# Kernel optimization log

Measured on AMD Instinct MI355X. Metric: run time of the kernel, lower is better.

Reference implementation:

```python
import jax, jax.numpy as jnp
import numpy as np

D_MODEL, D_STATE, D_CONV, EXPAND = 768, 16, 4, 2
D_INNER = EXPAND * D_MODEL        # 1536
DT_RANK = (D_MODEL + 15) // 16    # 48
B, L = 4, 1024
LN_EPS = 1e-5


def _causal_dw_conv(x, w, b):
    # x: [b,l,d], w: [d,k], b: [d] -- depthwise causal conv along l
    k = w.shape[1]
    xp = jnp.pad(x, ((0, 0), (k - 1, 0), (0, 0)))
    out = jnp.zeros_like(x)
    for i in range(k):  # k = 4, tiny fixed loop
        out = out + xp[:, i:i + x.shape[1], :] * w[:, i]
    return out + b


def _selective_scan(u, delta, A, Bm, Cm, Dp):
    # u, delta: [b,l,d]; A: [d,n]; Bm, Cm: [b,l,n]; Dp: [d]
    def step(h, inp):
        d_t, B_t, C_t, u_t = inp                         # [b,d],[b,n],[b,n],[b,d]
        dA = jnp.exp(d_t[:, :, None] * A)                # [b,d,n]
        h = dA * h + (d_t * u_t)[:, :, None] * B_t[:, None, :]
        return h, jnp.einsum('bdn,bn->bd', h, C_t)
    b, l, d = u.shape
    h0 = jnp.zeros((b, d, A.shape[1]), u.dtype)
    xs = (jnp.swapaxes(delta, 0, 1), jnp.swapaxes(Bm, 0, 1),
          jnp.swapaxes(Cm, 0, 1), jnp.swapaxes(u, 0, 1))
    _, ys = jax.lax.scan(step, h0, xs)                   # ys: [l,b,d]
    return jnp.swapaxes(ys, 0, 1) + u * Dp


def _mamba_dir(xz, conv_w, conv_bias, xp_w, dtp_w, dtp_bias, A_log, Dp):
    x, z = jnp.split(xz, 2, axis=-1)                     # each [b,l,d_inner]
    x = jax.nn.silu(_causal_dw_conv(x, conv_w, conv_bias))
    x_dbl = x @ xp_w.T                                   # [b,l,R+2N]
    dt, Bm, Cm = jnp.split(x_dbl, [DT_RANK, DT_RANK + D_STATE], axis=-1)
    dt = jax.nn.softplus(dt @ dtp_w.T + dtp_bias)        # [b,l,d_inner]
    A = -jnp.exp(A_log)                                  # [d_inner,n]
    y = _selective_scan(x, dt, A, Bm, Cm, Dp)
    return y * jax.nn.silu(z)


def _block_single(h, ln_w, ln_b, in_w, conv_w, conv_bias, xp_w, dtp_w, dtp_bias,
                  A_log, D_p, conv_w_b, conv_bias_b, xp_w_b, dtp_w_b, dtp_bias_b,
                  A_b_log, D_b, out_w):
    # LayerNorm
    mu = jnp.mean(h, -1, keepdims=True)
    var = jnp.mean(jnp.square(h - mu), -1, keepdims=True)
    hn = (h - mu) * jax.lax.rsqrt(var + LN_EPS) * ln_w + ln_b
    # Mamba (bimamba v2): shared in_proj/out_proj, fwd + flipped bwd scan
    xz = hn @ in_w.T                                     # [b,l,2*d_inner]
    out_f = _mamba_dir(xz, conv_w, conv_bias, xp_w, dtp_w, dtp_bias, A_log, D_p)
    out_b = _mamba_dir(xz[:, ::-1], conv_w_b, conv_bias_b, xp_w_b, dtp_w_b,
                       dtp_bias_b, A_b_log, D_b)
    return (out_f + out_b[:, ::-1]) @ out_w.T            # [b,l,d_model]


def setup_inputs() -> dict:
    key = jax.random.key(0)
    ks = iter(jax.random.split(key, 40))
    f = lambda *s: jax.random.normal(next(ks), s, jnp.float32)
    p = {}
    p['h_r'] = f(B, L, D_MODEL)
    p['h_i'] = f(B, L, D_MODEL)
    # leading axis 2 = (real-branch mamba_r, imag-branch mamba_i) parameters
    p['ln_w'] = jnp.ones((2, D_MODEL), jnp.float32)
    p['ln_b'] = jnp.zeros((2, D_MODEL), jnp.float32)
    p['in_w'] = f(2, 2 * D_INNER, D_MODEL) * 0.02
    a_init = jnp.broadcast_to(jnp.log(jnp.arange(1, D_STATE + 1, dtype=jnp.float32)),
                              (2, D_INNER, D_STATE))
    for pre in ('', 'b_'):
        sfx = '_b' if pre else ''
        p['conv_w' + sfx] = f(2, D_INNER, D_CONV) * 0.2
        p['conv_bias' + sfx] = f(2, D_INNER) * 0.02
        p['xp_w' + sfx] = f(2, DT_RANK + 2 * D_STATE, D_INNER) * 0.02
        p['dtp_w' + sfx] = f(2, D_INNER, DT_RANK) * 0.1
        p['dtp_bias' + sfx] = f(2, D_INNER) * 0.5
        p['A_log' + sfx if not pre else 'A_b_log'] = a_init
        p['D_p' + sfx if not pre else 'D_b'] = f(2, D_INNER) * 0.1
    p['out_w'] = f(2, D_MODEL, D_INNER) * 0.02
    return p


def reference(h_r, h_i, ln_w, ln_b, in_w, conv_w, conv_bias, xp_w, dtp_w,
              dtp_bias, A_log, D_p, conv_w_b, conv_bias_b, xp_w_b, dtp_w_b,
              dtp_bias_b, A_b_log, D_b, out_w):
    h = jnp.stack([h_r, h_i])                            # [2,b,l,d_model]
    out = jax.vmap(_block_single)(h, ln_w, ln_b, in_w, conv_w, conv_bias, xp_w,
                                  dtp_w, dtp_bias, A_log, D_p, conv_w_b,
                                  conv_bias_b, xp_w_b, dtp_w_b, dtp_bias_b,
                                  A_b_log, D_b, out_w)
    return (out[0], out[1])
```

## Files before the change

kernel.cpp:

```cpp
#include <hip/hip_runtime.h>
#include <hip/hip_bf16.h>
#include <math.h>


#define BB 4
#define LL 1024
#define DM 768
#define DI 1536
#define RK 48
#define NS 16
#define CH 32
#define CLEN 32
#define DB6 (DI / 256)
#define XSPLIT 4
#define XKC2 (DI / XSPLIT)

typedef __attribute__((ext_vector_type(8))) short bf16x8;
typedef __attribute__((ext_vector_type(4))) float f32x4;
typedef unsigned short us;
typedef unsigned int uns;

__device__ __forceinline__ float siluf(float x) {
    return x / (1.f + __expf(-x));
}
__device__ __forceinline__ float softplusf(float x) {
    return fmaxf(x, 0.f) + __logf(1.f + __expf(-fabsf(x)));
}
__device__ __forceinline__ us f2bf(float x) {
    __hip_bfloat16 h = __float2bfloat16(x);
    return *(us*)&h;
}
__device__ __forceinline__ float bf2f(uns v) {
    uns u = v << 16;
    return *(float*)&u;
}
__device__ __forceinline__ unsigned pack2bf(float a, float b) {
    return (unsigned)f2bf(a) | ((unsigned)f2bf(b) << 16);
}
__device__ __forceinline__ void async_cp16(const void* g, void* l) {
    __builtin_amdgcn_global_load_lds(
        (const __attribute__((address_space(1))) void*)g,
        (__attribute__((address_space(3))) void*)l, 16, 0, 0);
}
__device__ __forceinline__ void pow8s(float sc, float r, float* d) {
    float r2 = r * r, r3 = r2 * r, r4 = r2 * r2;
    d[0] = sc * r;   d[1] = sc * r2;  d[2] = d[1] * r;  d[3] = sc * r4;
    d[4] = d[3] * r; d[5] = d[3] * r2; d[6] = d[3] * r3; d[7] = d[3] * r4;
}

__global__ __launch_bounds__(256)
void zero_kernel(float4* __restrict__ p, int n4)
{
    int i = blockIdx.x * 256 + threadIdx.x;
    if (i < n4) p[i] = (float4){0.f, 0.f, 0.f, 0.f};
}

#define LNB (2 * BB * LL)
#define C1B ((2 * 2 * DI * DM) / 1024)
#define C2B ((2 * DM * DI) / 1024)
#define C3B ((2 * 80 * DI) / 1024)
__global__ __launch_bounds__(256)
void prep_kernel(const float* __restrict__ h_r, const float* __restrict__ h_i,
                 const float* __restrict__ ln_w, const float* __restrict__ ln_b,
                 const float* __restrict__ in_w, const float* __restrict__ out_w,
                 const float* __restrict__ xp_w, const float* __restrict__ xp_w_b,
                 us* __restrict__ hnb, us* __restrict__ wbi,
                 us* __restrict__ wbo, us* __restrict__ wbxf,
                 us* __restrict__ wbxb)
{
    int bid = blockIdx.x;
    int tid = threadIdx.x;

    if (bid < LNB) {
        int br = bid / (BB * LL);
        int row = bid % (BB * LL);
        const float* hsrc = br ? h_i : h_r;
        const float* w = ln_w + br * DM;
        const float* bvec = ln_b + br * DM;
        us* out = hnb + (size_t)br * BB * LL * DM;

        const float* x = hsrc + (size_t)row * DM;
        float v[3];
        float s = 0.f, s2 = 0.f;
#pragma unroll
        for (int j = 0; j < 3; ++j) {
            v[j] = x[tid + j * 256];
            s += v[j];
            s2 += v[j] * v[j];
        }
#pragma unroll
        for (int off = 32; off > 0; off >>= 1) {
            s += __shfl_down(s, off);
            s2 += __shfl_down(s2, off);
        }
        __shared__ float sw[4], sw2[4], stat[2];
        int wid = tid >> 6;
        if ((tid & 63) == 0) { sw[wid] = s; sw2[wid] = s2; }
        __syncthreads();
        if (tid == 0) {
            float a = sw[0] + sw[1] + sw[2] + sw[3];
            float a2 = sw2[0] + sw2[1] + sw2[2] + sw2[3];
            float mu = a * (1.f / DM);
            float var = a2 * (1.f / DM) - mu * mu;
            stat[0] = mu;
            stat[1] = rsqrtf(var + 1e-5f);
        }
        __syncthreads();
        float mu = stat[0], rs = stat[1];
        us* o = out + (size_t)row * DM;
#pragma unroll
        for (int j = 0; j < 3; ++j) {
            int i = tid + j * 256;
            o[i] = f2bf((v[j] - mu) * rs * w[i] + bvec[i]);
        }
        return;
    }
    bid -= LNB;

    const float* src;
    us* dst;
    if (bid < C1B)      { src = in_w;   dst = wbi; }
    else if ((bid -= C1B) < C2B) { src = out_w;  dst = wbo; }
    else if ((bid -= C2B) < C3B) { src = xp_w;   dst = wbxf; }
    else { bid -= C3B;    src = xp_w_b; dst = wbxb; }

    int i = (bid * 256 + tid) * 4;
    float4 v = *(const float4*)(src + i);
    dst[i + 0] = f2bf(v.x);
    dst[i + 1] = f2bf(v.y);
    dst[i + 2] = f2bf(v.z);
    dst[i + 3] = f2bf(v.w);
}

__global__ __launch_bounds__(256)
void gemm_mfma_bt(const us* __restrict__ hnb, const us* __restrict__ wbi,
                  us* __restrict__ XH, us* __restrict__ ZH)
{
    int br = blockIdx.z;
    const us* A = hnb + (size_t)br * BB * LL * DM;
    const us* B = wbi + (size_t)br * 2 * DI * DM;

    __shared__ us As[128 * 32];
    __shared__ us Bs[128 * 32];
    int tid = threadIdx.x;
    int wave = tid >> 6, lane = tid & 63;
    int wm = wave & 1, wn = wave >> 1;
    int quad = lane >> 4, lr = lane & 15;
    int m0 = blockIdx.y * 128, n0g = blockIdx.x * 128;

    us* C; int cn0;
    if (n0g < DI) { C = XH + (size_t)br * BB * LL * DI; cn0 = n0g; }
    else          { C = ZH + (size_t)br * BB * LL * DI; cn0 = n0g - DI; }

    f32x4 acc[4][4];
#pragma unroll
    for (int i = 0; i < 4; ++i)
#pragma unroll
        for (int j = 0; j < 4; ++j) acc[i][j] = (f32x4){0.f, 0.f, 0.f, 0.f};

    for (int kt = 0; kt < DM; kt += 32) {
#pragma unroll
        for (int i = 0; i < 2; ++i) {
            int idx = tid + i * 256;
            int row = idx >> 2, col = (idx & 3) * 8;
            async_cp16(A + (size_t)(m0 + row) * DM + kt + col, &As[idx * 8]);
            async_cp16(B + (size_t)(n0g + row) * DM + kt + col, &Bs[idx * 8]);
        }
        __syncthreads();

        bf16x8 af[4], bf[4];
#pragma unroll
        for (int mt = 0; mt < 4; ++mt)
            af[mt] = *(const bf16x8*)(&As[(wm * 64 + mt * 16 + lr) * 32 + quad * 8]);
#pragma unroll
        for (int nt = 0; nt < 4; ++nt)
            bf[nt] = *(const bf16x8*)(&Bs[(wn * 64 + nt * 16 + lr) * 32 + quad * 8]);
#pragma unroll
        for (int mt = 0; mt < 4; ++mt)
#pragma unroll
            for (int nt = 0; nt < 4; ++nt)
                acc[mt][nt] = __builtin_amdgcn_mfma_f32_16x16x32_bf16(
                    af[mt], bf[nt], acc[mt][nt], 0, 0, 0);
        __syncthreads();
    }

#pragma unroll
    for (int mt = 0; mt < 4; ++mt)
#pragma unroll
        for (int nt = 0; nt < 4; ++nt)
#pragma unroll
            for (int e = 0; e < 4; ++e) {
                int m = m0 + wm * 64 + mt * 16 + quad * 4 + e;
                int n = cn0 + wn * 64 + nt * 16 + lr;
                C[(size_t)m * DI + n] = f2bf(acc[mt][nt][e]);
            }
}

__global__ __launch_bounds__(256)
void gemm_mfma_bt64(const us* __restrict__ gb_all, const us* __restrict__ wbo,
                    float* __restrict__ out_all, int out_stride)
{
    int br = blockIdx.z;
    const us* A = gb_all + (size_t)br * BB * LL * DI;
    const us* B = wbo + (size_t)br * DM * DI;
    float* C = out_all + (size_t)br * out_stride;

    __shared__ us As[64 * 32];
    __shared__ us Bs[128 * 32];
    int tid = threadIdx.x;
    int wave = tid >> 6, lane = tid & 63;
    int wm = wave & 1, wn = wave >> 1;
    int quad = lane >> 4, lr = lane & 15;
    int m0 = blockIdx.y * 64, n0 = blockIdx.x * 128;

    f32x4 acc[2][4];
#pragma unroll
    for (int i = 0; i < 2; ++i)
#pragma unroll
        for (int j = 0; j < 4; ++j) acc[i][j] = (f32x4){0.f, 0.f, 0.f, 0.f};

    for (int kt = 0; kt < DI; kt += 32) {
        {
            int row = tid >> 2, col = (tid & 3) * 8;
            async_cp16(A + (size_t)(m0 + row) * DI + kt + col, &As[tid * 8]);
        }
#pragma unroll
        for (int i = 0; i < 2; ++i) {
            int idx = tid + i * 256;
            int row = idx >> 2, col = (idx & 3) * 8;
            async_cp16(B + (size_t)(n0 + row) * DI + kt + col, &Bs[idx * 8]);
        }
        __syncthreads();

        bf16x8 af[2], bf[4];
#pragma unroll
        for (int mt = 0; mt < 2; ++mt)
            af[mt] = *(const bf16x8*)(&As[(wm * 32 + mt * 16 + lr) * 32 + quad * 8]);
#pragma unroll
        for (int nt = 0; nt < 4; ++nt)
            bf[nt] = *(const bf16x8*)(&Bs[(wn * 64 + nt * 16 + lr) * 32 + quad * 8]);
#pragma unroll
        for (int mt = 0; mt < 2; ++mt)
#pragma unroll
            for (int nt = 0; nt < 4; ++nt)
                acc[mt][nt] = __builtin_amdgcn_mfma_f32_16x16x32_bf16(
                    af[mt], bf[nt], acc[mt][nt], 0, 0, 0);
        __syncthreads();
    }

#pragma unroll
    for (int mt = 0; mt < 2; ++mt)
#pragma unroll
        for (int nt = 0; nt < 4; ++nt)
#pragma unroll
            for (int e = 0; e < 4; ++e) {
                int m = m0 + wm * 32 + mt * 16 + quad * 4 + e;
                int n = n0 + wn * 64 + nt * 16 + lr;
                C[(size_t)m * DM + n] = acc[mt][nt][e];
            }
}

#define CT 32
#define CD 64
__device__ __forceinline__ float4 dw4(float4 x0, float4 x1, float4 x2, float4 x3,
                                      float4 wa, float4 wb, float4 wc, float4 wd,
                                      float4 cb)
{
    float4 o;
    o.x = cb.x + x0.x * wa.x + x1.x * wa.y + x2.x * wa.z + x3.x * wa.w;
    o.y = cb.y + x0.y * wb.x + x1.y * wb.y + x2.y * wb.z + x3.y * wb.w;
    o.z = cb.z + x0.z * wc.x + x1.z * wc.y + x2.z * wc.z + x3.z * wc.w;
    o.w = cb.w + x0.w * wd.x + x1.w * wd.y + x2.w * wd.z + x3.w * wd.w;
    return o;
}

__global__ __launch_bounds__(256)
void conv_fused(const us* __restrict__ XH,
                const float* __restrict__ conv_w, const float* __restrict__ conv_b,
                const float* __restrict__ conv_w_b, const float* __restrict__ conv_b_b,
                us* __restrict__ xc16)
{
    int zb = blockIdx.z;
    int br = zb / BB, b = zb % BB;
    const us* xz = XH + (size_t)br * BB * LL * DI;
    const float* wf = conv_w + (size_t)br * DI * 4;
    const float* cbf = conv_b + (size_t)br * DI;
    const float* wb = conv_w_b + (size_t)br * DI * 4;
    const float* cbb = conv_b_b + (size_t)br * DI;
    us* xcf16 = xc16 + (size_t)(br * 2 + 0) * BB * LL * DI;
    us* xcb16 = xc16 + (size_t)(br * 2 + 1) * BB * LL * DI;

    int d0 = blockIdx.x * CD;
    int s0 = blockIdx.y * CT;
    int tid = threadIdx.x;

    __shared__ float XT[CT + 6][CD + 4];

    for (int i = tid; i < (CT + 6) * (CD / 4); i += 256) {
        int r = i >> 4;
        int c4 = i & 15;
        int s = s0 - 3 + r;
        float4 v = (float4){0.f, 0.f, 0.f, 0.f};
        if (s >= 0 && s < LL) {
            uint2 w = *(const uint2*)(xz + ((size_t)(b * LL + s)) * DI
                                      + d0 + c4 * 4);
            v.x = bf2f(w.x & 0xffffu); v.y = bf2f(w.x >> 16);
            v.z = bf2f(w.y & 0xffffu); v.w = bf2f(w.y >> 16);
        }
        *(float4*)(&XT[r][c4 * 4]) = v;
    }

    int d4 = tid & 15;
    int sr = tid >> 4;
    int d = d0 + d4 * 4;
    float4 wf0 = *(const float4*)(wf + (size_t)(d + 0) * 4);
    float4 wf1 = *(const float4*)(wf + (size_t)(d + 1) * 4);
    float4 wf2 = *(const float4*)(wf + (size_t)(d + 2) * 4);
    float4 wf3 = *(const float4*)(wf + (size_t)(d + 3) * 4);
    float4 wb0 = *(const float4*)(wb + (size_t)(d + 0) * 4);
    float4 wb1 = *(const float4*)(wb + (size_t)(d + 1) * 4);
    float4 wb2 = *(const float4*)(wb + (size_t)(d + 2) * 4);
    float4 wb3 = *(const float4*)(wb + (size_t)(d + 3) * 4);
    float4 cf  = *(const float4*)(cbf + d);
    float4 cbv = *(const float4*)(cbb + d);
    __syncthreads();

    float4 x4[8];
#pragma unroll
    for (int j = 0; j < 8; ++j)
        x4[j] = *(const float4*)(&XT[2 * sr + j][d4 * 4]);

#pragma unroll
    for (int q = 0; q < 2; ++q) {
        int s = s0 + 2 * sr + q;
        float4 of = dw4(x4[q + 0], x4[q + 1], x4[q + 2], x4[q + 3],
                        wf0, wf1, wf2, wf3, cf);
        of.x = siluf(of.x); of.y = siluf(of.y);
        of.z = siluf(of.z); of.w = siluf(of.w);
        size_t fi = ((size_t)(b * LL + s)) * DI + d;
        uint2 pf; pf.x = pack2bf(of.x, of.y); pf.y = pack2bf(of.z, of.w);
        *(uint2*)(&xcf16[fi]) = pf;
        float4 ob = dw4(x4[q + 6], x4[q + 5], x4[q + 4], x4[q + 3],
                        wb0, wb1, wb2, wb3, cbv);
        ob.x = siluf(ob.x); ob.y = siluf(ob.y);
        ob.z = siluf(ob.z); ob.w = siluf(ob.w);
        size_t bi = ((size_t)(b * LL + (LL - 1 - s))) * DI + d;
        uint2 pb; pb.x = pack2bf(ob.x, ob.y); pb.y = pack2bf(ob.z, ob.w);
        *(uint2*)(&xcb16[bi]) = pb;
    }
}

__global__ __launch_bounds__(256)
void xproj_mfma(const us* __restrict__ xc16,
                const us* __restrict__ wbxf, const us* __restrict__ wbxb,
                float* __restrict__ xd)
{
    int z = blockIdx.z;
    int br = z >> 1, dir = z & 1;
    const us* A = xc16 + (size_t)z * BB * LL * DI;
    const us* W = (dir ? wbxb : wbxf) + (size_t)br * 80 * DI;
    float* out = xd + (size_t)z * BB * LL * 80;

    __shared__ us As[64 * 32];
    __shared__ us Ws[80 * 32];
    int tid = threadIdx.x;
    int wave = tid >> 6, lane = tid & 63;
    int quad = lane >> 4, lr = lane & 15;
    int m0 = blockIdx.y * 64;
    int k0 = blockIdx.x * XKC2;

    f32x4 acc[5];
#pragma unroll
    for (int j = 0; j < 5; ++j) acc[j] = (f32x4){0.f, 0.f, 0.f, 0.f};

    for (int kt = 0; kt < XKC2; kt += 32) {
        {
            int row = tid >> 2, col = (tid & 3) * 8;
            async_cp16(A + (size_t)(m0 + row) * DI + k0 + kt + col, &As[tid * 8]);
        }
        {
            int row = tid >> 2, col = (tid & 3) * 8;
            async_cp16(W + (size_t)row * DI + k0 + kt + col, &Ws[tid * 8]);
        }
        if (tid < 64) {
            int idx = 256 + tid;
            int row = idx >> 2, col = (idx & 3) * 8;
            async_cp16(W + (size_t)row * DI + k0 + kt + col, &Ws[idx * 8]);
        }
        __syncthreads();

        bf16x8 af = *(const bf16x8*)(&As[(wave * 16 + lr) * 32 + quad * 8]);
#pragma unroll
        for (int j = 0; j < 5; ++j) {
            bf16x8 bf = *(const bf16x8*)(&Ws[(j * 16 + lr) * 32 + quad * 8]);
            acc[j] = __builtin_amdgcn_mfma_f32_16x16x32_bf16(af, bf, acc[j], 0, 0, 0);
        }
        __syncthreads();
    }

#pragma unroll
    for (int j = 0; j < 5; ++j)
#pragma unroll
        for (int e = 0; e < 4; ++e) {
            int m = m0 + wave * 16 + quad * 4 + e;
            int n = j * 16 + lr;
            atomicAdd(&out[(size_t)m * 80 + n], acc[j][e]);
        }
}

__global__ __launch_bounds__(256)
void dtproj2(const float* __restrict__ xd,
             const float* __restrict__ dtp_w, const float* __restrict__ dtp_w_b,
             const float* __restrict__ dtp_bias, const float* __restrict__ dtp_bias_b,
             const us* __restrict__ xc16, uns* __restrict__ siB)
{
    int z = blockIdx.z;
    int br = z >> 1, dir = z & 1;
    const float* A = xd + (size_t)z * BB * LL * 80;
    const float* W = (dir ? dtp_w_b : dtp_w) + (size_t)br * DI * RK;
    const float* bias = (dir ? dtp_bias_b : dtp_bias) + (size_t)br * DI;
    const us* U = xc16 + (size_t)z * BB * LL * DI;
    uns* SI = siB + (size_t)z * BB * LL * DI;

    __shared__ float As[48][132];
    __shared__ float Ws[48][68];
    int tid = threadIdx.x;
    int m0 = blockIdx.y * 128, n0 = blockIdx.x * 64;

    for (int i = tid; i < 1536; i += 256) {
        int r = i / 12, kg = i % 12;
        float4 v = *(const float4*)(A + (size_t)(m0 + r) * 80 + kg * 4);
        As[kg * 4 + 0][r] = v.x; As[kg * 4 + 1][r] = v.y;
        As[kg * 4 + 2][r] = v.z; As[kg * 4 + 3][r] = v.w;
    }
    for (int i = tid; i < 768; i += 256) {
        int r = i / 12, kg = i % 12;
        float4 u = *(const float4*)(W + (size_t)(n0 + r) * RK + kg * 4);
        Ws[kg * 4 + 0][r] = u.x; Ws[kg * 4 + 1][r] = u.y;
        Ws[kg * 4 + 2][r] = u.z; Ws[kg * 4 + 3][r] = u.w;
    }
    __syncthreads();

    int tx = tid & 15, ty = tid >> 4;
    float acc[8][4];
#pragma unroll
    for (int i = 0; i < 8; ++i)
#pragma unroll
        for (int j = 0; j < 4; ++j) acc[i][j] = 0.f;

#pragma unroll 8
    for (int k = 0; k < RK; ++k) {
        float4 a0 = *(const float4*)(&As[k][ty * 4]);
        float4 a1 = *(const float4*)(&As[k][64 + ty * 4]);
        float4 w0 = *(const float4*)(&Ws[k][tx * 4]);
        float av[8], wv[4];
        av[0] = a0.x; av[1] = a0.y; av[2] = a0.z; av[3] = a0.w;
        av[4] = a1.x; av[5] = a1.y; av[6] = a1.z; av[7] = a1.w;
        wv[0] = w0.x; wv[1] = w0.y; wv[2] = w0.z; wv[3] = w0.w;
#pragma unroll
        for (int i = 0; i < 8; ++i)
#pragma unroll
            for (int j = 0; j < 4; ++j)
                acc[i][j] += av[i] * wv[j];
    }

    float4 bv = *(const float4*)(bias + n0 + tx * 4);
#pragma unroll
    for (int i = 0; i < 8; ++i) {
        int m = m0 + ((i & 4) ? 64 : 0) + ty * 4 + (i & 3);
        float4 o;
        o.x = softplusf(acc[i][0] + bv.x);
        o.y = softplusf(acc[i][1] + bv.y);
        o.z = softplusf(acc[i][2] + bv.z);
        o.w = softplusf(acc[i][3] + bv.w);
        size_t off = (size_t)m * DI + n0 + tx * 4;
        uint2 up = *(const uint2*)(U + off);
        uint4 s;
        s.x = (uns)f2bf(o.x) | ((up.x & 0xffffu) << 16);
        s.y = (uns)f2bf(o.y) | (up.x & 0xffff0000u);
        s.z = (uns)f2bf(o.z) | ((up.y & 0xffffu) << 16);
        s.w = (uns)f2bf(o.w) | (up.y & 0xffff0000u);
        *(uint4*)(SI + off) = s;
    }
}

__device__ __forceinline__ bool a_is_canonical8(const float* Alog, int d, int half)
{
    bool ok = true;
    const float4* a4 = (const float4*)(Alog + (size_t)d * NS + half * 8);
#pragma unroll
    for (int j = 0; j < 2; ++j) {
        float4 v = a4[j];
        float b0 = (float)(half * 8 + 4 * j + 1), b1 = (float)(half * 8 + 4 * j + 2);
        float b2 = (float)(half * 8 + 4 * j + 3), b3 = (float)(half * 8 + 4 * j + 4);
        ok = ok && (fabsf(__expf(v.x) - b0) < 1e-3f * b0)
                && (fabsf(__expf(v.y) - b1) < 1e-3f * b1)
                && (fabsf(__expf(v.z) - b2) < 1e-3f * b2)
                && (fabsf(__expf(v.w) - b3) < 1e-3f * b3);
    }
    return ok;
}

__global__ __launch_bounds__(512)
void scan_p1_b(const uns* __restrict__ siB, const float* __restrict__ xd,
               const float* __restrict__ A_log, const float* __restrict__ A_b_log,
               uns* __restrict__ PQall)
{
    int z = blockIdx.z;
    int br = z >> 1, dir = z & 1;
    const uns* SI = siB + (size_t)z * BB * LL * DI;
    const float* xdbl = xd + (size_t)z * BB * LL * 80;
    const float* Alog = (dir ? A_b_log : A_log) + (size_t)br * DI * NS;
    uns* PQ = PQall + (size_t)z * CH * BB * DI * NS;

    int c = blockIdx.y;
    int b = blockIdx.x / DB6;
    int dblk = (blockIdx.x % DB6) * 256;
    int tid = threadIdx.x;
    int dl = tid >> 1, half = tid & 1;
    int d = dblk + dl;
    int wave = tid >> 6, lane = tid & 63;

    bool afast = a_is_canonical8(Alog, d, half);

    __shared__ float Bs[CLEN * NS];
    __shared__ uns DU[2][8][256];
    for (int i = tid; i < CLEN * NS; i += 512) {
        int t = i >> 4, n = i & 15;
        Bs[i] = xdbl[((size_t)(b * LL + c * CLEN + t)) * 80 + 48 + n];
    }

    size_t rowbase = ((size_t)b * LL + c * CLEN) * DI + dblk;
#define STAGE_S(s, dbuf)                                                   \
    async_cp16(SI + rowbase + (size_t)((s) * 8 + wave) * DI + lane * 4,    \
               &DU[dbuf][wave][lane * 4]);

    STAGE_S(0, 0);

    float q[8];
#pragma unroll
    for (int n = 0; n < 8; ++n) q[n] = 0.f;
    float dtsum = 0.f;

    if (afast) {
#pragma unroll
        for (int s = 0; s < 4; ++s) {
            __syncthreads();
            if (s < 3) STAGE_S(s + 1, (s + 1) & 1);
            int buf = s & 1;
#pragma unroll
            for (int t8 = 0; t8 < 8; ++t8) {
                uns pk = DU[buf][t8][dl];
                float dtv = bf2f(pk & 0xffffu), uv = bf2f(pk >> 16);
                float du = dtv * uv;
                dtsum += dtv;
                float r = __expf(-dtv);
                float sc = 1.f;
                if (half) { float r2 = r * r, r4 = r2 * r2; sc = r4 * r4; }
                float dA[8];
                pow8s(sc, r, dA);
                const float4* b4 = (const float4*)(Bs + (s * 8 + t8) * NS + half * 8);
                float4 B0 = b4[0], B1 = b4[1];
                q[0] = dA[0] * q[0] + du * B0.x;
                q[1] = dA[1] * q[1] + du * B0.y;
                q[2] = dA[2] * q[2] + du * B0.z;
                q[3] = dA[3] * q[3] + du * B0.w;
                q[4] = dA[4] * q[4] + du * B1.x;
                q[5] = dA[5] * q[5] + du * B1.y;
                q[6] = dA[6] * q[6] + du * B1.z;
                q[7] = dA[7] * q[7] + du * B1.w;
            }
        }
        float rs = __expf(-dtsum);
        float sc = 1.f;
        if (half) { float r2 = rs * rs, r4 = r2 * r2; sc = r4 * r4; }
        float P[8];
        pow8s(sc, rs, P);
        uns* o = PQ + (size_t)c * (BB * DI * NS) + (size_t)(b * DI + d) * NS
               + half * 8;
        uint4 s0, s1;
        s0.x = pack2bf(P[0], q[0]); s0.y = pack2bf(P[1], q[1]);
        s0.z = pack2bf(P[2], q[2]); s0.w = pack2bf(P[3], q[3]);
        s1.x = pack2bf(P[4], q[4]); s1.y = pack2bf(P[5], q[5]);
        s1.z = pack2bf(P[6], q[6]); s1.w = pack2bf(P[7], q[7]);
        *(uint4*)(o) = s0;
        *(uint4*)(o + 4) = s1;
    } else {
        float Av[8];
        {
            const float4* a4 = (const float4*)(Alog + (size_t)d * NS + half * 8);
#pragma unroll
            for (int j = 0; j < 2; ++j) {
                float4 v = a4[j];
                Av[4 * j + 0] = -__expf(v.x); Av[4 * j + 1] = -__expf(v.y);
                Av[4 * j + 2] = -__expf(v.z); Av[4 * j + 3] = -__expf(v.w);
            }
        }
#pragma unroll
        for (int s = 0; s < 4; ++s) {
            __syncthreads();
            if (s < 3) STAGE_S(s + 1, (s + 1) & 1);
            int buf = s & 1;
#pragma unroll
            for (int t8 = 0; t8 < 8; ++t8) {
                uns pk = DU[buf][t8][dl];
                float dtv = bf2f(pk & 0xffffu), uv = bf2f(pk >> 16);
                float du = dtv * uv;
                dtsum += dtv;
                const float4* b4 = (const float4*)(Bs + (s * 8 + t8) * NS + half * 8);
                float4 B0 = b4[0], B1 = b4[1];
                q[0] = __expf(dtv * Av[0]) * q[0] + du * B0.x;
                q[1] = __expf(dtv * Av[1]) * q[1] + du * B0.y;
                q[2] = __expf(dtv * Av[2]) * q[2] + du * B0.z;
                q[3] = __expf(dtv * Av[3]) * q[3] + du * B0.w;
                q[4] = __expf(dtv * Av[4]) * q[4] + du * B1.x;
                q[5] = __expf(dtv * Av[5]) * q[5] + du * B1.y;
                q[6] = __expf(dtv * Av[6]) * q[6] + du * B1.z;
                q[7] = __expf(dtv * Av[7]) * q[7] + du * B1.w;
            }
        }
        uns* o = PQ + (size_t)c * (BB * DI * NS) + (size_t)(b * DI + d) * NS
               + half * 8;
#pragma unroll
        for (int n = 0; n < 8; ++n)
            o[n] = pack2bf(__expf(dtsum * Av[n]), q[n]);
    }
#undef STAGE_S
}

__global__ __launch_bounds__(256)
void scan_mid_b(uns* __restrict__ PQall)
{
    int z = blockIdx.z;
    uns* PQ = PQall + (size_t)z * CH * BB * DI * NS;
    int gid = blockIdx.x * 256 + threadIdx.x;
    const size_t stride = (size_t)(BB * DI * NS);
    uns pr[4];
#pragma unroll
    for (int i = 0; i < 4; ++i) pr[i] = PQ[(size_t)i * stride + gid];
    float h = 0.f;
    for (int c = 0; c < CH; ++c) {
        uns s = pr[c & 3];
        if (c + 4 < CH) pr[c & 3] = PQ[(size_t)(c + 4) * stride + gid];
        float P = bf2f(s & 0xffffu), q = bf2f(s >> 16);
        PQ[(size_t)c * stride + gid] = (s & 0xffff0000u) | (uns)f2bf(h);
        h = P * h + q;
    }
}

__global__ __launch_bounds__(512)
void scan_p2_b(const uns* __restrict__ siB, const float* __restrict__ xd,
               const float* __restrict__ A_log, const float* __restrict__ A_b_log,
               const float* __restrict__ D_p, const float* __restrict__ D_b,
               const uns* __restrict__ PQall, us* __restrict__ gall)
{
    int z = blockIdx.z;
    int br = z >> 1, dir = z & 1;
    const uns* SI = siB + (size_t)z * BB * LL * DI;
    const float* xdbl = xd + (size_t)z * BB * LL * 80;
    const float* Alog = (dir ? A_b_log : A_log) + (size_t)br * DI * NS;
    const float* Dp = (dir ? D_b : D_p) + (size_t)br * DI;
    const uns* PQ = PQall + (size_t)z * CH * BB * DI * NS;
    us* g = gall + (size_t)z * BB * LL * DI;
    int rev = dir;

    int c = blockIdx.y;
    int b = blockIdx.x / DB6;
    int dblk = (blockIdx.x % DB6) * 256;
    int tid = threadIdx.x;
    int dl = tid >> 1, half = tid & 1;
    int d = dblk + dl;
    int wave = tid >> 6, lane = tid & 63;

    bool afast = a_is_canonical8(Alog, d, half);

    float h[8];
    {
        const uns* h2 = PQ + (size_t)c * (BB * DI * NS)
                        + (size_t)(b * DI + d) * NS + half * 8;
        uint4 a = *(const uint4*)(h2);
        uint4 bq = *(const uint4*)(h2 + 4);
        h[0] = bf2f(a.x & 0xffffu); h[1] = bf2f(a.y & 0xffffu);
        h[2] = bf2f(a.z & 0xffffu); h[3] = bf2f(a.w & 0xffffu);
        h[4] = bf2f(bq.x & 0xffffu); h[5] = bf2f(bq.y & 0xffffu);
        h[6] = bf2f(bq.z & 0xffffu); h[7] = bf2f(bq.w & 0xffffu);
    }
    float Dpv = Dp[d];

    __shared__ float Bs[CLEN * NS];
    __shared__ float Cs[CLEN * NS];
    __shared__ uns DU[2][8][256];
    for (int i = tid; i < CLEN * NS; i += 512) {
        int t = i >> 4, n = i & 15;
        size_t src = ((size_t)(b * LL + c * CLEN + t)) * 80;
        Bs[i] = xdbl[src + 48 + n];
        Cs[i] = xdbl[src + 64 + n];
    }

    size_t rowbase = ((size_t)b * LL + c * CLEN) * DI + dblk;
#define STAGE_S(s, dbuf)                                                   \
    async_cp16(SI + rowbase + (size_t)((s) * 8 + wave) * DI + lane * 4,    \
               &DU[dbuf][wave][lane * 4]);

    STAGE_S(0, 0);

    size_t gbase = (size_t)b * LL * DI + d;

    if (afast) {
#pragma unroll
        for (int s = 0; s < 4; ++s) {
            __syncthreads();
            if (s < 3) STAGE_S(s + 1, (s + 1) & 1);
            int buf = s & 1;
#pragma unroll
            for (int t8 = 0; t8 < 8; ++t8) {
                uns pk = DU[buf][t8][dl];
                float dtv = bf2f(pk & 0xffffu), uv = bf2f(pk >> 16);
                float du = dtv * uv;
                float r = __expf(-dtv);
                float sc = 1.f;
                if (half) { float r2 = r * r, r4 = r2 * r2; sc = r4 * r4; }
                float dA[8];
                pow8s(sc, r, dA);
                int t = s * 8 + t8;
                const float4* b4 = (const float4*)(Bs + t * NS + half * 8);
                const float4* c4 = (const float4*)(Cs + t * NS + half * 8);
                float4 B0 = b4[0], B1 = b4[1];
                float4 C0 = c4[0], C1 = c4[1];
                float y = 0.f;
                h[0] = dA[0] * h[0] + du * B0.x; y += h[0] * C0.x;
                h[1] = dA[1] * h[1] + du * B0.y; y += h[1] * C0.y;
                h[2] = dA[2] * h[2] + du * B0.z; y += h[2] * C0.z;
                h[3] = dA[3] * h[3] + du * B0.w; y += h[3] * C0.w;
                h[4] = dA[4] * h[4] + du * B1.x; y += h[4] * C1.x;
                h[5] = dA[5] * h[5] + du * B1.y; y += h[5] * C1.y;
                h[6] = dA[6] * h[6] + du * B1.z; y += h[6] * C1.z;
                h[7] = dA[7] * h[7] + du * B1.w; y += h[7] * C1.w;
                y += __shfl_xor(y, 1);
                if (half == 0) {
                    int tt = c * CLEN + t;
                    int ot = rev ? (LL - 1 - tt) : tt;
                    g[gbase + (size_t)ot * DI] = f2bf(y + uv * Dpv);
                }
            }
        }
    } else {
        float Av[8];
        {
            const float4* a4 = (const float4*)(Alog + (size_t)d * NS + half * 8);
#pragma unroll
            for (int j = 0; j < 2; ++j) {
                float4 v = a4[j];
                Av[4 * j + 0] = -__expf(v.x); Av[4 * j + 1] = -__expf(v.y);
                Av[4 * j + 2] = -__expf(v.z); Av[4 * j + 3] = -__expf(v.w);
            }
        }
#pragma unroll
        for (int s = 0; s < 4; ++s) {
            __syncthreads();
            if (s < 3) STAGE_S(s + 1, (s + 1) & 1);
            int buf = s & 1;
#pragma unroll
            for (int t8 = 0; t8 < 8; ++t8) {
                uns pk = DU[buf][t8][dl];
                float dtv = bf2f(pk & 0xffffu), uv = bf2f(pk >> 16);
                float du = dtv * uv;
                int t = s * 8 + t8;
                const float4* b4 = (const float4*)(Bs + t * NS + half * 8);
                const float4* c4 = (const float4*)(Cs + t * NS + half * 8);
                float4 B0 = b4[0], B1 = b4[1];
                float4 C0 = c4[0], C1 = c4[1];
                float y = 0.f;
                h[0] = __expf(dtv * Av[0]) * h[0] + du * B0.x; y += h[0] * C0.x;
                h[1] = __expf(dtv * Av[1]) * h[1] + du * B0.y; y += h[1] * C0.y;
                h[2] = __expf(dtv * Av[2]) * h[2] + du * B0.z; y += h[2] * C0.z;
                h[3] = __expf(dtv * Av[3]) * h[3] + du * B0.w; y += h[3] * C0.w;
                h[4] = __expf(dtv * Av[4]) * h[4] + du * B1.x; y += h[4] * C1.x;
                h[5] = __expf(dtv * Av[5]) * h[5] + du * B1.y; y += h[5] * C1.y;
                h[6] = __expf(dtv * Av[6]) * h[6] + du * B1.z; y += h[6] * C1.z;
                h[7] = __expf(dtv * Av[7]) * h[7] + du * B1.w; y += h[7] * C1.w;
                y += __shfl_xor(y, 1);
                if (half == 0) {
                    int tt = c * CLEN + t;
                    int ot = rev ? (LL - 1 - tt) : tt;
                    g[gbase + (size_t)ot * DI] = f2bf(y + uv * Dpv);
                }
            }
        }
    }
#undef STAGE_S
}

__global__ __launch_bounds__(256)
void gate2_kernel(const us* __restrict__ gall, const us* __restrict__ ZH,
                  us* __restrict__ gb_all)
{
    int br = blockIdx.z;
    const us* g0 = gall + (size_t)(br * 2 + 0) * BB * LL * DI;
    const us* g1 = gall + (size_t)(br * 2 + 1) * BB * LL * DI;
    const us* zh = ZH + (size_t)br * BB * LL * DI;
    us* gb = gb_all + (size_t)br * BB * LL * DI;

    int gid = (blockIdx.x * 256 + threadIdx.x) * 4;
    uint2 zz = *(const uint2*)(zh + gid);
    uint2 a = *(const uint2*)(g0 + gid);
    uint2 bb = *(const uint2*)(g1 + gid);
    float z0 = bf2f(zz.x & 0xffffu), z1 = bf2f(zz.x >> 16);
    float z2 = bf2f(zz.y & 0xffffu), z3 = bf2f(zz.y >> 16);
    float v0 = (bf2f(a.x & 0xffffu) + bf2f(bb.x & 0xffffu)) * siluf(z0);
    float v1 = (bf2f(a.x >> 16)     + bf2f(bb.x >> 16))     * siluf(z1);
    float v2 = (bf2f(a.y & 0xffffu) + bf2f(bb.y & 0xffffu)) * siluf(z2);
    float v3 = (bf2f(a.y >> 16)     + bf2f(bb.y >> 16))     * siluf(z3);
    uint2 o; o.x = pack2bf(v0, v1); o.y = pack2bf(v2, v3);
    *(uint2*)(gb + gid) = o;
}

extern "C" void kernel_launch(void* const* d_in, const int* in_sizes, int n_in,
                              void* d_out, int out_size, void* d_ws, size_t ws_size,
                              hipStream_t stream)
{
    const float* h_r        = (const float*)d_in[0];
    const float* h_i        = (const float*)d_in[1];
    const float* ln_w       = (const float*)d_in[2];
    const float* ln_b       = (const float*)d_in[3];
    const float* in_w       = (const float*)d_in[4];
    const float* conv_w     = (const float*)d_in[5];
    const float* conv_bias  = (const float*)d_in[6];
    const float* xp_w       = (const float*)d_in[7];
    const float* dtp_w      = (const float*)d_in[8];
    const float* dtp_bias   = (const float*)d_in[9];
    const float* A_log      = (const float*)d_in[10];
    const float* D_p        = (const float*)d_in[11];
    const float* conv_w_b   = (const float*)d_in[12];
    const float* conv_bias_b= (const float*)d_in[13];
    const float* xp_w_b     = (const float*)d_in[14];
    const float* dtp_w_b    = (const float*)d_in[15];
    const float* dtp_bias_b = (const float*)d_in[16];
    const float* A_b_log    = (const float*)d_in[17];
    const float* D_b        = (const float*)d_in[18];
    const float* out_w      = (const float*)d_in[19];
    float* out = (float*)d_out;

    const size_t E = (size_t)BB * LL * DI;
    const size_t XD = (size_t)BB * LL * 80;
    const size_t PQN = (size_t)CH * BB * DI * NS;

    char* p = (char*)d_ws;
    auto alloc = [&](size_t bytes) {
        char* r = p;
        p += (bytes + 255) & ~(size_t)255;
        return r;
    };
    uns* siB   = (uns*)alloc(4 * E * 4);
    us* hnb    = (us*)siB;
    us* XH     = (us*)alloc(2 * E * 2);
    float* xd  = (float*)XH;
    us* ZH     = (us*)alloc(2 * E * 2);
    us* xc16   = (us*)alloc(4 * E * 2);
    us* gall   = xc16;
    uns* PQ    = (uns*)alloc(4 * PQN * 4);
    us* gb     = (us*)PQ;
    us* wbi    = (us*)alloc((size_t)2 * 2 * DI * DM * 2);
    us* wbo    = (us*)alloc((size_t)2 * DM * DI * 2);
    us* wbxf   = (us*)alloc((size_t)2 * 80 * DI * 2);
    us* wbxb   = (us*)alloc((size_t)2 * 80 * DI * 2);
    (void)ws_size;

    prep_kernel<<<LNB + C1B + C2B + 2 * C3B, 256, 0, stream>>>(
        h_r, h_i, ln_w, ln_b, in_w, out_w, xp_w, xp_w_b,
        hnb, wbi, wbo, wbxf, wbxb);

    gemm_mfma_bt<<<dim3((2 * DI) / 128, (BB * LL) / 128, 2), 256, 0, stream>>>(
        hnb, wbi, XH, ZH);

    conv_fused<<<dim3(DI / CD, LL / CT, 2 * BB), 256, 0, stream>>>(
        XH, conv_w, conv_bias, conv_w_b, conv_bias_b, xc16);

    zero_kernel<<<(int)(4 * XD / 4 + 255) / 256, 256, 0, stream>>>(
        (float4*)xd, (int)(4 * XD / 4));

    xproj_mfma<<<dim3(XSPLIT, (BB * LL) / 64, 4), 256, 0, stream>>>(
        xc16, wbxf, wbxb, xd);

    dtproj2<<<dim3(DI / 64, (BB * LL) / 128, 4), 256, 0, stream>>>(
        xd, dtp_w, dtp_w_b, dtp_bias, dtp_bias_b, xc16, siB);

    scan_p1_b<<<dim3(BB * DB6, CH, 4), 512, 0, stream>>>(
        siB, xd, A_log, A_b_log, PQ);

    scan_mid_b<<<dim3((int)((BB * DI * NS) / 256), 1, 4), 256, 0, stream>>>(PQ);

    scan_p2_b<<<dim3(BB * DB6, CH, 4), 512, 0, stream>>>(
        siB, xd, A_log, A_b_log, D_p, D_b, PQ, gall);

    gate2_kernel<<<dim3((int)(E / 1024), 1, 2), 256, 0, stream>>>(
        gall, ZH, gb);

    gemm_mfma_bt64<<<dim3(DM / 128, (BB * LL) / 64, 2), 256, 0, stream>>>(
        gb, wbo, out, (int)((size_t)BB * LL * DM));
}
```

Measured before the change: 492.0 us.

## Fold xdbl zeroing into prep kernel and use fewer, longer scan chunks

Zeroing of the x_proj accumulation buffer moves out of its own launch and into the prep kernel as extra blocks. To make that possible the buffer gets its own workspace allocation instead of aliasing XH, which the conv kernel still reads after prep runs. Separately, the chunked selective scan now uses 16 chunks of 64 steps instead of 32 chunks of 32. This halves the per-chunk state traffic and mid-pass work but lengthens the serial loop per block and halves the grid parallelism of the scan passes.

```diff
diff --git a/kernel.cpp b/kernel.cpp
--- a/kernel.cpp
+++ b/kernel.cpp
@@ -9,8 +9,8 @@
 #define DI 1536
 #define RK 48
 #define NS 16
-#define CH 32
-#define CLEN 32
+#define CH 16
+#define CLEN 64
 #define DB6 (DI / 256)
 #define XSPLIT 4
 #define XKC2 (DI / XSPLIT)
@@ -48,17 +48,11 @@
     d[4] = d[3] * r; d[5] = d[3] * r2; d[6] = d[3] * r3; d[7] = d[3] * r4;
 }
 
-__global__ __launch_bounds__(256)
-void zero_kernel(float4* __restrict__ p, int n4)
-{
-    int i = blockIdx.x * 256 + threadIdx.x;
-    if (i < n4) p[i] = (float4){0.f, 0.f, 0.f, 0.f};
-}
-
 #define LNB (2 * BB * LL)
 #define C1B ((2 * 2 * DI * DM) / 1024)
 #define C2B ((2 * DM * DI) / 1024)
 #define C3B ((2 * 80 * DI) / 1024)
+#define ZXDB ((4 * BB * LL * 80) / 1024)
 __global__ __launch_bounds__(256)
 void prep_kernel(const float* __restrict__ h_r, const float* __restrict__ h_i,
                  const float* __restrict__ ln_w, const float* __restrict__ ln_b,
@@ -66,7 +60,7 @@
                  const float* __restrict__ xp_w, const float* __restrict__ xp_w_b,
                  us* __restrict__ hnb, us* __restrict__ wbi,
                  us* __restrict__ wbo, us* __restrict__ wbxf,
-                 us* __restrict__ wbxb)
+                 us* __restrict__ wbxb, float4* __restrict__ xdz)
 {
     int bid = blockIdx.x;
     int tid = threadIdx.x;
@@ -119,10 +113,15 @@
 
     const float* src;
     us* dst;
-    if (bid < C1B)      { src = in_w;   dst = wbi; }
+    if (bid < C1B)               { src = in_w;   dst = wbi; }
     else if ((bid -= C1B) < C2B) { src = out_w;  dst = wbo; }
     else if ((bid -= C2B) < C3B) { src = xp_w;   dst = wbxf; }
-    else { bid -= C3B;    src = xp_w_b; dst = wbxb; }
+    else if ((bid -= C3B) < C3B) { src = xp_w_b; dst = wbxb; }
+    else {
+        bid -= C3B;
+        xdz[bid * 256 + tid] = (float4){0.f, 0.f, 0.f, 0.f};
+        return;
+    }
 
     int i = (bid * 256 + tid) * 4;
     float4 v = *(const float4*)(src + i);
@@ -544,9 +543,9 @@
 
     if (afast) {
 #pragma unroll
-        for (int s = 0; s < 4; ++s) {
+        for (int s = 0; s < CLEN / 8; ++s) {
             __syncthreads();
-            if (s < 3) STAGE_S(s + 1, (s + 1) & 1);
+            if (s < CLEN / 8 - 1) STAGE_S(s + 1, (s + 1) & 1);
             int buf = s & 1;
 #pragma unroll
             for (int t8 = 0; t8 < 8; ++t8) {
@@ -597,9 +596,9 @@
             }
         }
 #pragma unroll
-        for (int s = 0; s < 4; ++s) {
+        for (int s = 0; s < CLEN / 8; ++s) {
             __syncthreads();
-            if (s < 3) STAGE_S(s + 1, (s + 1) & 1);
+            if (s < CLEN / 8 - 1) STAGE_S(s + 1, (s + 1) & 1);
             int buf = s & 1;
 #pragma unroll
             for (int t8 = 0; t8 < 8; ++t8) {
@@ -708,9 +707,9 @@
 
     if (afast) {
 #pragma unroll
-        for (int s = 0; s < 4; ++s) {
+        for (int s = 0; s < CLEN / 8; ++s) {
             __syncthreads();
-            if (s < 3) STAGE_S(s + 1, (s + 1) & 1);
+            if (s < CLEN / 8 - 1) STAGE_S(s + 1, (s + 1) & 1);
             int buf = s & 1;
 #pragma unroll
             for (int t8 = 0; t8 < 8; ++t8) {
@@ -756,9 +755,9 @@
             }
         }
 #pragma unroll
-        for (int s = 0; s < 4; ++s) {
+        for (int s = 0; s < CLEN / 8; ++s) {
             __syncthreads();
-            if (s < 3) STAGE_S(s + 1, (s + 1) & 1);
+            if (s < CLEN / 8 - 1) STAGE_S(s + 1, (s + 1) & 1);
             int buf = s & 1;
 #pragma unroll
             for (int t8 = 0; t8 < 8; ++t8) {
@@ -854,21 +853,21 @@
     uns* siB   = (uns*)alloc(4 * E * 4);
     us* hnb    = (us*)siB;
     us* XH     = (us*)alloc(2 * E * 2);
-    float* xd  = (float*)XH;
     us* ZH     = (us*)alloc(2 * E * 2);
     us* xc16   = (us*)alloc(4 * E * 2);
     us* gall   = xc16;
     uns* PQ    = (uns*)alloc(4 * PQN * 4);
     us* gb     = (us*)PQ;
+    float* xd  = (float*)alloc(4 * XD * 4);
     us* wbi    = (us*)alloc((size_t)2 * 2 * DI * DM * 2);
     us* wbo    = (us*)alloc((size_t)2 * DM * DI * 2);
     us* wbxf   = (us*)alloc((size_t)2 * 80 * DI * 2);
     us* wbxb   = (us*)alloc((size_t)2 * 80 * DI * 2);
     (void)ws_size;
 
-    prep_kernel<<<LNB + C1B + C2B + 2 * C3B, 256, 0, stream>>>(
+    prep_kernel<<<LNB + C1B + C2B + 2 * C3B + ZXDB, 256, 0, stream>>>(
         h_r, h_i, ln_w, ln_b, in_w, out_w, xp_w, xp_w_b,
-        hnb, wbi, wbo, wbxf, wbxb);
+        hnb, wbi, wbo, wbxf, wbxb, (float4*)xd);
 
     gemm_mfma_bt<<<dim3((2 * DI) / 128, (BB * LL) / 128, 2), 256, 0, stream>>>(
         hnb, wbi, XH, ZH);
@@ -876,9 +875,6 @@
     conv_fused<<<dim3(DI / CD, LL / CT, 2 * BB), 256, 0, stream>>>(
         XH, conv_w, conv_bias, conv_w_b, conv_bias_b, xc16);
 
-    zero_kernel<<<(int)(4 * XD / 4 + 255) / 256, 256, 0, stream>>>(
-        (float4*)xd, (int)(4 * XD / 4));
-
     xproj_mfma<<<dim3(XSPLIT, (BB * LL) / 64, 4), 256, 0, stream>>>(
         xc16, wbxf, wbxb, xd);
 
```

Result: faster. 476.5 us (-3.2%).
